# Performance work log

Hardware: AMD Instinct MI355X
Metric: run time of the kernel (lower is better)

Reference implementation:

```python
import jax, jax.numpy as jnp
import numpy as np

B, T, N, P = 64, 288, 1024, 12


def setup_inputs() -> dict:
    key = jax.random.key(0)
    k1, k2 = jax.random.split(key)
    x = jax.random.normal(k1, (B, T, N, 1), dtype=jnp.float32)
    # scale AR coefficients so the self-feeding recurrence stays numerically stable
    ar_params = jax.random.normal(k2, (N, P), dtype=jnp.float32) * 0.05
    bias = jnp.zeros((N,), dtype=jnp.float32)
    return {"x": x, "ar_params": ar_params, "bias": bias}


def reference(x, ar_params, bias):
    # x: (B, T, N, 1); ar_params: (N, p); bias: (N,)
    Bd, Td, Nd, _ = x.shape
    p = ar_params.shape[1]
    # initial history window = last p entries of the full input series per (b, n)
    h0 = jnp.transpose(x[:, Td - p:, :, 0], (0, 2, 1))  # (B, N, p)

    def step(h, _):
        # per-node AR(p): dot of node coefficients with its rolling history
        pred = jnp.einsum('np,bnp->bn', ar_params, h) + bias  # (B, N)
        h = jnp.concatenate([h[:, :, 1:], pred[:, :, None]], axis=-1)
        return h, pred

    _, preds = jax.lax.scan(step, h0, None, length=Td)  # (T, B, N)
    return jnp.transpose(preds, (1, 0, 2))[..., None]  # (B, T, N, 1)
```

## Files before the change

kernel.cpp:

```cpp
#include <hip/hip_runtime.h>


constexpr int B = 64;
constexpr int T = 288;
constexpr int N = 1024;
constexpr int P = 12;

__global__ __launch_bounds__(256) void ar_model_kernel(
    const float* __restrict__ x,
    const float* __restrict__ ar,
    const float* __restrict__ bias,
    float* __restrict__ out)
{
    const int tid = blockIdx.x * blockDim.x + threadIdx.x;
    const int n = tid & (N - 1);
    const int b = tid >> 10;
    if (b >= B) return;

    float a[P];
    const float* arow = ar + n * P;
#pragma unroll
    for (int j = 0; j < P; ++j) a[j] = arow[j];
    const float bs = bias[n];

    float acc[P];
#pragma unroll
    for (int s = 0; s < P; ++s) acc[s] = bs;

    const float* xb = x + (size_t)b * T * N + (size_t)(T - P) * N + n;
#pragma unroll
    for (int i = 0; i < P; ++i) {
        const float hv = xb[(size_t)i * N];
#pragma unroll
        for (int t = 0; t <= i; ++t)
            acc[t] = fmaf(a[i - t], hv, acc[t]);
    }

    float* ob = out + (size_t)b * T * N + n;

#pragma unroll 1
    for (int tt = 0; tt < T; tt += P) {
#pragma unroll
        for (int k = 0; k < P; ++k) {
            const float pred = acc[k];
            ob[(size_t)(tt + k) * N] = pred;
            acc[k] = fmaf(a[0], pred, bs);
#pragma unroll
            for (int d = 1; d < P; ++d)
                acc[(k + d) % P] = fmaf(a[P - d], pred, acc[(k + d) % P]);
        }
    }
}

extern "C" void kernel_launch(void* const* d_in, const int* in_sizes, int n_in,
                              void* d_out, int out_size, void* d_ws, size_t ws_size,
                              hipStream_t stream) {
    const float* x    = (const float*)d_in[0];
    const float* ar   = (const float*)d_in[1];
    const float* bias = (const float*)d_in[2];
    float* out = (float*)d_out;

    const int total = B * N;
    const int block = 256;
    const int grid = (total + block - 1) / block;
    ar_model_kernel<<<grid, block, 0, stream>>>(x, ar, bias, out);
}
```

Baseline: 118.6 us.

## Precompute linear AR impulse responses and apply them as a parallel matvec

Because the recurrence is linear, each output equals a per-node linear combination of the initial 12-value history plus a bias term. One kernel runs the recurrence once per unit basis vector and once for the bias, writing weight tables W and Beta into the workspace. A second kernel computes every output in parallel over time and batch chunks from those tables. This removes the long serial 288-step dependency chain across only 64K threads, at the cost of roughly 14 MB of extra workspace traffic and a second launch. The propagate kernel itself is still serial over T, with about 13K threads.

```diff
diff --git a/kernel.cpp b/kernel.cpp
--- a/kernel.cpp
+++ b/kernel.cpp
@@ -5,28 +5,114 @@
 constexpr int T = 288;
 constexpr int N = 1024;
 constexpr int P = 12;
+constexpr int BC = 8;
+constexpr int TC = 8;
+
+__global__ __launch_bounds__(256) void ar_propagate_kernel(
+    const float* __restrict__ ar,
+    const float* __restrict__ bias,
+    float* __restrict__ W,
+    float* __restrict__ Beta)
+{
+    const int tid = blockIdx.x * blockDim.x + threadIdx.x;
+    const int n = tid & (N - 1);
+    const int seq = tid >> 10;
+    if (seq > P) return;
+
+    float a[P];
+    const float* arow = ar + n * P;
+#pragma unroll
+    for (int j = 0; j < P; ++j) a[j] = arow[j];
+
+    const bool is_beta = (seq == P);
+    const float bs = is_beta ? bias[n] : 0.0f;
+
+    float acc[P];
+#pragma unroll
+    for (int s = 0; s < P; ++s) acc[s] = bs;
+
+#pragma unroll
+    for (int i = 0; i < P; ++i) {
+        const float hv = (i == seq) ? 1.0f : 0.0f;
+#pragma unroll
+        for (int t = 0; t <= i; ++t)
+            acc[t] = fmaf(a[i - t], hv, acc[t]);
+    }
+
+    float* obase = is_beta ? (Beta + n) : (W + (size_t)seq * N + n);
+    const size_t ostride = is_beta ? (size_t)N : (size_t)P * N;
+
+#pragma unroll 1
+    for (int tt = 0; tt < T; tt += P) {
+#pragma unroll
+        for (int k = 0; k < P; ++k) {
+            const float pred = acc[k];
+            obase[(size_t)(tt + k) * ostride] = pred;
+            acc[k] = fmaf(a[0], pred, bs);
+#pragma unroll
+            for (int d = 1; d < P; ++d)
+                acc[(k + d) % P] = fmaf(a[P - d], pred, acc[(k + d) % P]);
+        }
+    }
+}
+
+__global__ __launch_bounds__(256) void ar_apply_kernel(
+    const float* __restrict__ x,
+    const float* __restrict__ W,
+    const float* __restrict__ Beta,
+    float* __restrict__ out)
+{
+    const int bid = blockIdx.x;
+    const int nt = bid & 3;
+    const int tt = (bid >> 2) % (T / TC);
+    const int bt = bid / (4 * (T / TC));
+    const int n = nt * 256 + threadIdx.x;
+    const int t0 = tt * TC;
+    const int b0 = bt * BC;
+
+    float xw[BC][P];
+#pragma unroll
+    for (int i = 0; i < BC; ++i) {
+        const float* xb = x + ((size_t)(b0 + i) * T + (T - P)) * N + n;
+#pragma unroll
+        for (int j = 0; j < P; ++j)
+            xw[i][j] = xb[(size_t)j * N];
+    }
+
+#pragma unroll 2
+    for (int t = 0; t < TC; ++t) {
+        float w[P];
+        const float* wrow = W + (size_t)(t0 + t) * P * N + n;
+#pragma unroll
+        for (int j = 0; j < P; ++j) w[j] = wrow[(size_t)j * N];
+        const float bb = Beta[(size_t)(t0 + t) * N + n];
+#pragma unroll
+        for (int i = 0; i < BC; ++i) {
+            float acc = bb;
+#pragma unroll
+            for (int j = 0; j < P; ++j)
+                acc = fmaf(w[j], xw[i][j], acc);
+            out[((size_t)(b0 + i) * T + (t0 + t)) * N + n] = acc;
+        }
+    }
+}
 
 __global__ __launch_bounds__(256) void ar_model_kernel(
-    const float* __restrict__ x,
-    const float* __restrict__ ar,
-    const float* __restrict__ bias,
-    float* __restrict__ out)
+    const float* __restrict__ x, const float* __restrict__ ar,
+    const float* __restrict__ bias, float* __restrict__ out)
 {
     const int tid = blockIdx.x * blockDim.x + threadIdx.x;
     const int n = tid & (N - 1);
     const int b = tid >> 10;
     if (b >= B) return;
-
     float a[P];
     const float* arow = ar + n * P;
 #pragma unroll
     for (int j = 0; j < P; ++j) a[j] = arow[j];
     const float bs = bias[n];
-
     float acc[P];
 #pragma unroll
     for (int s = 0; s < P; ++s) acc[s] = bs;
-
     const float* xb = x + (size_t)b * T * N + (size_t)(T - P) * N + n;
 #pragma unroll
     for (int i = 0; i < P; ++i) {
@@ -35,9 +121,7 @@
         for (int t = 0; t <= i; ++t)
             acc[t] = fmaf(a[i - t], hv, acc[t]);
     }
-
     float* ob = out + (size_t)b * T * N + n;
-
 #pragma unroll 1
     for (int tt = 0; tt < T; tt += P) {
 #pragma unroll
@@ -60,8 +144,17 @@
     const float* bias = (const float*)d_in[2];
     float* out = (float*)d_out;
 
-    const int total = B * N;
-    const int block = 256;
-    const int grid = (total + block - 1) / block;
-    ar_model_kernel<<<grid, block, 0, stream>>>(x, ar, bias, out);
+    const size_t w_elems = (size_t)T * P * N;
+    const size_t beta_elems = (size_t)T * N;
+    const size_t need = (w_elems + beta_elems) * sizeof(float);
+
+    if (ws_size >= need) {
+        float* W = (float*)d_ws;
+        float* Beta = W + w_elems;
+        ar_propagate_kernel<<<(13 * N) / 256, 256, 0, stream>>>(ar, bias, W, Beta);
+        ar_apply_kernel<<<4 * (T / TC) * (B / BC), 256, 0, stream>>>(x, W, Beta, out);
+    } else {
+        const int total = B * N;
+        ar_model_kernel<<<(total + 255) / 256, 256, 0, stream>>>(x, ar, bias, out);
+    }
 }
```

Measured after the change: 142.2 us. +19.9%, slower.

## Split AR recurrence into checkpoint pass and parallel chunked recompute

Applied to the files above, without the earlier changes.

A first kernel runs the recurrence with no output stores and saves the 12-value history at every 48-step chunk boundary into workspace. A second kernel launches one thread per (chunk, batch, node), restarts from the checkpoint and writes its chunk, which gives six times more parallel threads for the store-heavy phase. The price is recomputing most of the recurrence, an extra launch, and a workspace round trip. If the workspace is too small, the original kernel is used.

```diff
diff --git a/kernel.cpp b/kernel.cpp
--- a/kernel.cpp
+++ b/kernel.cpp
@@ -5,12 +5,19 @@
 constexpr int T = 288;
 constexpr int N = 1024;
 constexpr int P = 12;
+constexpr int CHUNK = 48;
+constexpr int NCHUNK = T / CHUNK;
+constexpr int NCKPT = NCHUNK - 1;
 
-__global__ __launch_bounds__(256) void ar_model_kernel(
+#define SCATTER_PROLOGUE(acc, a, hv, i)                                        \
+  _Pragma("unroll") for (int _t = 0; _t <= (i); ++_t)                          \
+      acc[_t] = fmaf(a[(i) - _t], (hv), acc[_t]);
+
+__global__ __launch_bounds__(256) void ar_ckpt_kernel(
     const float* __restrict__ x,
     const float* __restrict__ ar,
     const float* __restrict__ bias,
-    float* __restrict__ out)
+    float* __restrict__ ws)
 {
     const int tid = blockIdx.x * blockDim.x + threadIdx.x;
     const int n = tid & (N - 1);
@@ -31,13 +38,113 @@
 #pragma unroll
     for (int i = 0; i < P; ++i) {
         const float hv = xb[(size_t)i * N];
-#pragma unroll
-        for (int t = 0; t <= i; ++t)
-            acc[t] = fmaf(a[i - t], hv, acc[t]);
+        SCATTER_PROLOGUE(acc, a, hv, i)
     }
 
+#pragma unroll 1
+    for (int tt = 0; tt < T - CHUNK; tt += P) {
+        float pr[P];
+#pragma unroll
+        for (int k = 0; k < P; ++k) {
+            const float pred = acc[k];
+            pr[k] = pred;
+            acc[k] = fmaf(a[0], pred, bs);
+#pragma unroll
+            for (int d = 1; d < P; ++d)
+                acc[(k + d) % P] = fmaf(a[P - d], pred, acc[(k + d) % P]);
+        }
+        if ((tt % CHUNK) == CHUNK - P) {
+            const int c = tt / CHUNK;
+            float4* dst = (float4*)(ws + ((size_t)c * B * N + tid) * P);
+            dst[0] = make_float4(pr[0], pr[1], pr[2], pr[3]);
+            dst[1] = make_float4(pr[4], pr[5], pr[6], pr[7]);
+            dst[2] = make_float4(pr[8], pr[9], pr[10], pr[11]);
+        }
+    }
+}
+
+__global__ __launch_bounds__(256) void ar_chunk_kernel(
+    const float* __restrict__ x,
+    const float* __restrict__ ar,
+    const float* __restrict__ bias,
+    const float* __restrict__ ws,
+    float* __restrict__ out)
+{
+    const int tid = blockIdx.x * blockDim.x + threadIdx.x;
+    const int n = tid & (N - 1);
+    const int bn = tid & (B * N - 1);
+    const int b = (tid >> 10) & (B - 1);
+    const int c = tid / (B * N);
+    if (c >= NCHUNK) return;
+
+    float a[P];
+    const float* arow = ar + n * P;
+#pragma unroll
+    for (int j = 0; j < P; ++j) a[j] = arow[j];
+    const float bs = bias[n];
+
+    float acc[P];
+#pragma unroll
+    for (int s = 0; s < P; ++s) acc[s] = bs;
+
+    if (c == 0) {
+        const float* xb = x + (size_t)b * T * N + (size_t)(T - P) * N + n;
+#pragma unroll
+        for (int i = 0; i < P; ++i) {
+            const float hv = xb[(size_t)i * N];
+            SCATTER_PROLOGUE(acc, a, hv, i)
+        }
+    } else {
+        const float4* src =
+            (const float4*)(ws + ((size_t)(c - 1) * B * N + bn) * P);
+        const float4 v0 = src[0], v1 = src[1], v2 = src[2];
+        const float hw[P] = {v0.x, v0.y, v0.z, v0.w, v1.x, v1.y,
+                             v1.z, v1.w, v2.x, v2.y, v2.z, v2.w};
+#pragma unroll
+        for (int i = 0; i < P; ++i) {
+            const float hv = hw[i];
+            SCATTER_PROLOGUE(acc, a, hv, i)
+        }
+    }
+
+    float* ob = out + (size_t)b * T * N + (size_t)c * CHUNK * N + n;
+#pragma unroll 1
+    for (int tt = 0; tt < CHUNK; tt += P) {
+#pragma unroll
+        for (int k = 0; k < P; ++k) {
+            const float pred = acc[k];
+            ob[(size_t)(tt + k) * N] = pred;
+            acc[k] = fmaf(a[0], pred, bs);
+#pragma unroll
+            for (int d = 1; d < P; ++d)
+                acc[(k + d) % P] = fmaf(a[P - d], pred, acc[(k + d) % P]);
+        }
+    }
+}
+
+__global__ __launch_bounds__(256) void ar_model_kernel(
+    const float* __restrict__ x, const float* __restrict__ ar,
+    const float* __restrict__ bias, float* __restrict__ out)
+{
+    const int tid = blockIdx.x * blockDim.x + threadIdx.x;
+    const int n = tid & (N - 1);
+    const int b = tid >> 10;
+    if (b >= B) return;
+    float a[P];
+    const float* arow = ar + n * P;
+#pragma unroll
+    for (int j = 0; j < P; ++j) a[j] = arow[j];
+    const float bs = bias[n];
+    float acc[P];
+#pragma unroll
+    for (int s = 0; s < P; ++s) acc[s] = bs;
+    const float* xb = x + (size_t)b * T * N + (size_t)(T - P) * N + n;
+#pragma unroll
+    for (int i = 0; i < P; ++i) {
+        const float hv = xb[(size_t)i * N];
+        SCATTER_PROLOGUE(acc, a, hv, i)
+    }
     float* ob = out + (size_t)b * T * N + n;
-
 #pragma unroll 1
     for (int tt = 0; tt < T; tt += P) {
 #pragma unroll
@@ -60,8 +167,14 @@
     const float* bias = (const float*)d_in[2];
     float* out = (float*)d_out;
 
-    const int total = B * N;
-    const int block = 256;
-    const int grid = (total + block - 1) / block;
-    ar_model_kernel<<<grid, block, 0, stream>>>(x, ar, bias, out);
+    const size_t need = (size_t)NCKPT * B * N * P * sizeof(float);
+
+    if (ws_size >= need) {
+        float* ws = (float*)d_ws;
+        ar_ckpt_kernel<<<(B * N) / 256, 256, 0, stream>>>(x, ar, bias, ws);
+        ar_chunk_kernel<<<(B * N * NCHUNK) / 256, 256, 0, stream>>>(
+            x, ar, bias, ws, out);
+    } else {
+        ar_model_kernel<<<(B * N) / 256, 256, 0, stream>>>(x, ar, bias, out);
+    }
 }
```

New measurement: 135.7 us. 14.5% more time.

## Split time axis into chunks with redundant recurrence replay for more parallelism

Applied to the files above, without the earlier changes.

The launch grows to four times as many threads, one per (chunk, batch, node). Each thread replays the AR recurrence without storing until it reaches its chunk's start, then writes only its 72 output steps. Before, only one block per CU was resident, so there was little latency hiding for the serial recurrence and the strided stores. The cost is about 2.5x more total FMA work, and the critical path for the last chunk still covers all 288 steps.

```diff
diff --git a/kernel.cpp b/kernel.cpp
--- a/kernel.cpp
+++ b/kernel.cpp
@@ -5,8 +5,10 @@
 constexpr int T = 288;
 constexpr int N = 1024;
 constexpr int P = 12;
+constexpr int CHUNK = 72;
+constexpr int NCHUNK = T / CHUNK;
 
-__global__ __launch_bounds__(256) void ar_model_kernel(
+__global__ __launch_bounds__(256) void ar_chunked_kernel(
     const float* __restrict__ x,
     const float* __restrict__ ar,
     const float* __restrict__ bias,
@@ -14,8 +16,8 @@
 {
     const int tid = blockIdx.x * blockDim.x + threadIdx.x;
     const int n = tid & (N - 1);
-    const int b = tid >> 10;
-    if (b >= B) return;
+    const int b = (tid >> 10) & (B - 1);
+    const int c = tid >> 16;
 
     float a[P];
     const float* arow = ar + n * P;
@@ -36,10 +38,22 @@
             acc[t] = fmaf(a[i - t], hv, acc[t]);
     }
 
-    float* ob = out + (size_t)b * T * N + n;
+    const int skip = c * CHUNK;
+#pragma unroll 1
+    for (int tt = 0; tt < skip; tt += P) {
+#pragma unroll
+        for (int k = 0; k < P; ++k) {
+            const float pred = acc[k];
+            acc[k] = fmaf(a[0], pred, bs);
+#pragma unroll
+            for (int d = 1; d < P; ++d)
+                acc[(k + d) % P] = fmaf(a[P - d], pred, acc[(k + d) % P]);
+        }
+    }
 
+    float* ob = out + (size_t)b * T * N + (size_t)skip * N + n;
 #pragma unroll 1
-    for (int tt = 0; tt < T; tt += P) {
+    for (int tt = 0; tt < CHUNK; tt += P) {
 #pragma unroll
         for (int k = 0; k < P; ++k) {
             const float pred = acc[k];
@@ -60,8 +74,6 @@
     const float* bias = (const float*)d_in[2];
     float* out = (float*)d_out;
 
-    const int total = B * N;
-    const int block = 256;
-    const int grid = (total + block - 1) / block;
-    ar_model_kernel<<<grid, block, 0, stream>>>(x, ar, bias, out);
+    const int total = B * N * NCHUNK;
+    ar_chunked_kernel<<<total / 256, 256, 0, stream>>>(x, ar, bias, out);
 }
```

Result: slower. 126.4 us (+6.6%).
